# Kernel tuning notes

Measured on AMD Instinct MI355X. Metric: run time of the kernel, lower is better.

The kernel has to match this reference:

```python
import jax, jax.numpy as jnp
import numpy as np

N, NTIMES, D_FEAT = 2048, 32, 128


def setup_inputs() -> dict:
    key = jax.random.key(0)
    k1, k2 = jax.random.split(key)
    return {
        "target_fairness": jnp.zeros((), dtype=jnp.float32),
        "prediction": jax.random.uniform(k1, (N, NTIMES), dtype=jnp.float32),
        "X_distance": jax.random.normal(k2, (N, D_FEAT), dtype=jnp.float32),
        "ntimes": NTIMES,
        "scale": jnp.ones((), dtype=jnp.float32),
    }


def reference(target_fairness, prediction, X_distance, ntimes, scale):
    n = prediction.shape[0]
    # cosine distance matrix: 1 - cos_sim, matches sklearn cosine_distances
    norms = jnp.linalg.norm(X_distance, axis=1, keepdims=True)
    Xn = X_distance / norms
    dist = 1.0 - Xn @ Xn.T  # [N, N]
    # pairwise |pred_j - pred_k| over all time points: [N, N, T]
    diff = jnp.abs(prediction[:, None, :] - prediction[None, :, :])
    hinge = jnp.maximum(0.0, diff - scale * dist[:, :, None])
    # only pairs k > j contribute
    mask = jnp.triu(jnp.ones((n, n), dtype=bool), k=1)
    R_beta = jnp.sum(jnp.where(mask[:, :, None], hinge, 0.0))
    model_fairness = 2.0 * R_beta / (n * (n - 1) * ntimes)
    return jnp.maximum(0.0, model_fairness - target_fairness)
```

## Files before the change

kernel.cpp:

```cpp
#include <hip/hip_runtime.h>

#define N 2048
#define T 32
#define D 128
#define BT 32
#define MT (N / BT)
#define NTILES (MT * (MT + 1) / 2)
#define STR 36

#define LGKM0() __builtin_amdgcn_s_waitcnt(0xc07f)

__global__ __launch_bounds__(64) void pair_kernel(
    const float* __restrict__ pred,
    const float* __restrict__ X,
    const float* __restrict__ scale_p,
    double* __restrict__ partials) {
  __shared__ float SA[BT * STR], SB[BT * STR];
  __shared__ float nrmA[BT], nrmB[BT];

  const int t = blockIdx.x;
  int a = (int)((2 * MT + 1 -
                 sqrtf((float)((2 * MT + 1) * (2 * MT + 1) - 8 * t))) * 0.5f);
  while (a > 0 && t < a * MT - a * (a - 1) / 2) --a;
  while (t >= (a + 1) * MT - (a + 1) * a / 2) ++a;
  const int b = a + (t - (a * MT - a * (a - 1) / 2));

  const int tid  = threadIdx.x;
  const int srow = tid >> 1;
  const int co   = (tid & 1) << 4;
  const int aRow0 = a * BT, bRow0 = b * BT;
  const float scale = scale_p[0];

  const float* xar = X + (size_t)(aRow0 + srow) * D + co;
  const float* xbr = X + (size_t)(bRow0 + srow) * D + co;

  const int tx = tid & 7, ty = tid >> 3;
  float dot[4][4];
#pragma unroll
  for (int i = 0; i < 4; ++i)
#pragma unroll
    for (int l = 0; l < 4; ++l) dot[i][l] = 0.0f;
  float ssA = 0.0f, ssB = 0.0f;

  for (int dc = 0; dc < 4; ++dc) {
#pragma unroll
    for (int j = 0; j < 4; ++j) {
      float4 va = *(const float4*)(xar + dc * 32 + 4 * j);
      float4 vb = *(const float4*)(xbr + dc * 32 + 4 * j);
      ssA += va.x * va.x + va.y * va.y + va.z * va.z + va.w * va.w;
      ssB += vb.x * vb.x + vb.y * vb.y + vb.z * vb.z + vb.w * vb.w;
      *(float4*)(&SA[srow * STR + co + 4 * j]) = va;
      *(float4*)(&SB[srow * STR + co + 4 * j]) = vb;
    }
    LGKM0();
#pragma unroll
    for (int d4 = 0; d4 < 8; ++d4) {
      float4 a4[4], b4[4];
#pragma unroll
      for (int i = 0; i < 4; ++i) {
        a4[i] = *(const float4*)(&SA[(ty + 8 * i) * STR + d4 * 4]);
        b4[i] = *(const float4*)(&SB[(tx + 8 * i) * STR + d4 * 4]);
      }
#pragma unroll
      for (int i = 0; i < 4; ++i)
#pragma unroll
        for (int l = 0; l < 4; ++l)
          dot[i][l] += a4[i].x * b4[l].x + a4[i].y * b4[l].y +
                       a4[i].z * b4[l].z + a4[i].w * b4[l].w;
    }
  }

  ssA += __shfl_xor(ssA, 1, 64);
  ssB += __shfl_xor(ssB, 1, 64);
  if ((tid & 1) == 0) {
    nrmA[srow] = rsqrtf(ssA);
    nrmB[srow] = rsqrtf(ssB);
  }

  {
    const float* par = pred + (size_t)(aRow0 + srow) * T + co;
    const float* pbr = pred + (size_t)(bRow0 + srow) * T + co;
#pragma unroll
    for (int j = 0; j < 4; ++j) {
      *(float4*)(&SA[srow * STR + co + 4 * j]) = *(const float4*)(par + 4 * j);
      *(float4*)(&SB[srow * STR + co + 4 * j]) = *(const float4*)(pbr + 4 * j);
    }
  }
  LGKM0();

  float na[4], nb[4];
#pragma unroll
  for (int i = 0; i < 4; ++i) {
    na[i] = nrmA[ty + 8 * i];
    nb[i] = nrmB[tx + 8 * i];
  }
  float ps[4][4];
#pragma unroll
  for (int i = 0; i < 4; ++i)
#pragma unroll
    for (int l = 0; l < 4; ++l) {
      dot[i][l] = scale * (1.0f - dot[i][l] * na[i] * nb[l]);
      ps[i][l]  = 0.0f;
    }

#pragma unroll
  for (int t4 = 0; t4 < 8; ++t4) {
    float4 qa[4], qb[4];
#pragma unroll
    for (int i = 0; i < 4; ++i) {
      qa[i] = *(const float4*)(&SA[(ty + 8 * i) * STR + t4 * 4]);
      qb[i] = *(const float4*)(&SB[(tx + 8 * i) * STR + t4 * 4]);
    }
#pragma unroll
    for (int i = 0; i < 4; ++i)
#pragma unroll
      for (int l = 0; l < 4; ++l) {
        float s = dot[i][l];
        ps[i][l] += fmaxf(fabsf(qa[i].x - qb[l].x), s) +
                    fmaxf(fabsf(qa[i].y - qb[l].y), s) +
                    fmaxf(fabsf(qa[i].z - qb[l].z), s) +
                    fmaxf(fabsf(qa[i].w - qb[l].w), s);
      }
  }

  float tsum = 0.0f;
  const bool offdiag = (b > a);
#pragma unroll
  for (int i = 0; i < 4; ++i)
#pragma unroll
    for (int l = 0; l < 4; ++l) {
      int jy = ty + 8 * i, kx = tx + 8 * l;
      bool valid = offdiag || (kx > jy);
      tsum += valid ? (ps[i][l] - 32.0f * dot[i][l]) : 0.0f;
    }

  double dsum = (double)tsum;
#pragma unroll
  for (int off = 32; off > 0; off >>= 1) dsum += __shfl_down(dsum, off, 64);
  if (tid == 0) partials[blockIdx.x] = dsum;
}

__global__ __launch_bounds__(256) void finalize_kernel(
    const double* __restrict__ partials, const float* __restrict__ target,
    float* __restrict__ out) {
  __shared__ double red[4];
  double s = 0.0;
  for (int i = threadIdx.x; i < NTILES; i += 256) s += partials[i];
#pragma unroll
  for (int off = 32; off > 0; off >>= 1) s += __shfl_down(s, off, 64);
  int wave = threadIdx.x >> 6, lane = threadIdx.x & 63;
  if (lane == 0) red[wave] = s;
  __syncthreads();
  if (threadIdx.x == 0) {
    double tot = red[0] + red[1] + red[2] + red[3];
    double mf  = 2.0 * tot / ((double)N * (double)(N - 1) * (double)T);
    double r   = mf - (double)target[0];
    out[0] = (float)(r > 0.0 ? r : 0.0);
  }
}

extern "C" void kernel_launch(void* const* d_in, const int* in_sizes, int n_in,
                              void* d_out, int out_size, void* d_ws, size_t ws_size,
                              hipStream_t stream) {
  const float* target = (const float*)d_in[0];
  const float* pred   = (const float*)d_in[1];
  const float* X      = (const float*)d_in[2];
  const float* scale  = (const float*)d_in[4];

  double* partials = (double*)d_ws;

  pair_kernel<<<dim3(NTILES), dim3(64), 0, stream>>>(pred, X, scale, partials);
  finalize_kernel<<<dim3(1), dim3(256), 0, stream>>>(partials, target,
                                                     (float*)d_out);
}
```

Measured before the change: 97.50 us.

## Compute cosine Gram tile with split-bf16 MFMA instead of scalar FMA

Replaces the LDS-staged scalar FP32 dot-product loop for the 32x32 Gram tile with MFMA 16x16x32 bf16 instructions. Each value is split into high and low bf16 parts, and three products (hh, hl, lh) approximate FP32 accuracy. X is read directly from global memory into registers, so the LDS staging and its waits for the feature matrix are gone. The hinge loop is remapped to the MFMA output layout. This trades some dot-product precision and three times the MFMA count for far fewer scalar FMAs.

```diff
diff --git a/kernel.cpp b/kernel.cpp
--- a/kernel.cpp
+++ b/kernel.cpp
@@ -8,14 +8,33 @@
 #define NTILES (MT * (MT + 1) / 2)
 #define STR 36
 
+typedef float floatx4 __attribute__((ext_vector_type(4)));
+typedef short bf16x8 __attribute__((ext_vector_type(8)));
+
 #define LGKM0() __builtin_amdgcn_s_waitcnt(0xc07f)
+
+__device__ __forceinline__ void split8(float4 a, float4 b, bf16x8& h, bf16x8& l) {
+  float v[8] = {a.x, a.y, a.z, a.w, b.x, b.y, b.z, b.w};
+#pragma unroll
+  for (int i = 0; i < 8; ++i) {
+    unsigned u = __float_as_uint(v[i]);
+    h[i] = (short)(u >> 16);
+    float lo = v[i] - __uint_as_float(u & 0xffff0000u);
+    l[i] = (short)(__float_as_uint(lo) >> 16);
+  }
+}
+
+__device__ __forceinline__ float sumsq8(float4 a, float4 b) {
+  return a.x * a.x + a.y * a.y + a.z * a.z + a.w * a.w +
+         b.x * b.x + b.y * b.y + b.z * b.z + b.w * b.w;
+}
 
 __global__ __launch_bounds__(64) void pair_kernel(
     const float* __restrict__ pred,
     const float* __restrict__ X,
     const float* __restrict__ scale_p,
     double* __restrict__ partials) {
-  __shared__ float SA[BT * STR], SB[BT * STR];
+  __shared__ float Pa[BT * STR], Pb[BT * STR];
   __shared__ float nrmA[BT], nrmB[BT];
 
   const int t = blockIdx.x;
@@ -26,113 +45,125 @@
   const int b = a + (t - (a * MT - a * (a - 1) / 2));
 
   const int tid  = threadIdx.x;
-  const int srow = tid >> 1;
-  const int co   = (tid & 1) << 4;
+  const int m    = tid & 15;
+  const int quad = tid >> 4;
   const int aRow0 = a * BT, bRow0 = b * BT;
   const float scale = scale_p[0];
 
-  const float* xar = X + (size_t)(aRow0 + srow) * D + co;
-  const float* xbr = X + (size_t)(bRow0 + srow) * D + co;
-
-  const int tx = tid & 7, ty = tid >> 3;
-  float dot[4][4];
-#pragma unroll
-  for (int i = 0; i < 4; ++i)
-#pragma unroll
-    for (int l = 0; l < 4; ++l) dot[i][l] = 0.0f;
-  float ssA = 0.0f, ssB = 0.0f;
-
-  for (int dc = 0; dc < 4; ++dc) {
-#pragma unroll
-    for (int j = 0; j < 4; ++j) {
-      float4 va = *(const float4*)(xar + dc * 32 + 4 * j);
-      float4 vb = *(const float4*)(xbr + dc * 32 + 4 * j);
-      ssA += va.x * va.x + va.y * va.y + va.z * va.z + va.w * va.w;
-      ssB += vb.x * vb.x + vb.y * vb.y + vb.z * vb.z + vb.w * vb.w;
-      *(float4*)(&SA[srow * STR + co + 4 * j]) = va;
-      *(float4*)(&SB[srow * STR + co + 4 * j]) = vb;
-    }
-    LGKM0();
-#pragma unroll
-    for (int d4 = 0; d4 < 8; ++d4) {
-      float4 a4[4], b4[4];
-#pragma unroll
-      for (int i = 0; i < 4; ++i) {
-        a4[i] = *(const float4*)(&SA[(ty + 8 * i) * STR + d4 * 4]);
-        b4[i] = *(const float4*)(&SB[(tx + 8 * i) * STR + d4 * 4]);
-      }
-#pragma unroll
-      for (int i = 0; i < 4; ++i)
-#pragma unroll
-        for (int l = 0; l < 4; ++l)
-          dot[i][l] += a4[i].x * b4[l].x + a4[i].y * b4[l].y +
-                       a4[i].z * b4[l].z + a4[i].w * b4[l].w;
-    }
-  }
-
-  ssA += __shfl_xor(ssA, 1, 64);
-  ssB += __shfl_xor(ssB, 1, 64);
-  if ((tid & 1) == 0) {
-    nrmA[srow] = rsqrtf(ssA);
-    nrmB[srow] = rsqrtf(ssB);
-  }
-
   {
+    const int srow = tid >> 1, co = (tid & 1) << 4;
     const float* par = pred + (size_t)(aRow0 + srow) * T + co;
     const float* pbr = pred + (size_t)(bRow0 + srow) * T + co;
 #pragma unroll
     for (int j = 0; j < 4; ++j) {
-      *(float4*)(&SA[srow * STR + co + 4 * j]) = *(const float4*)(par + 4 * j);
-      *(float4*)(&SB[srow * STR + co + 4 * j]) = *(const float4*)(pbr + 4 * j);
+      *(float4*)(&Pa[srow * STR + co + 4 * j]) = *(const float4*)(par + 4 * j);
+      *(float4*)(&Pb[srow * STR + co + 4 * j]) = *(const float4*)(pbr + 4 * j);
     }
   }
+
+  floatx4 acc[2][2];
+#pragma unroll
+  for (int I = 0; I < 2; ++I)
+#pragma unroll
+    for (int J = 0; J < 2; ++J) acc[I][J] = (floatx4){0.f, 0.f, 0.f, 0.f};
+  float ssA[2] = {0.f, 0.f}, ssB[2] = {0.f, 0.f};
+
+  const float* xa0 = X + (size_t)(aRow0 + m) * D + quad * 8;
+  const float* xb0 = X + (size_t)(bRow0 + m) * D + quad * 8;
+
+#pragma unroll
+  for (int ks = 0; ks < 4; ++ks) {
+    bf16x8 hA[2], lA[2], hB[2], lB[2];
+#pragma unroll
+    for (int I = 0; I < 2; ++I) {
+      float4 u0 = *(const float4*)(xa0 + (size_t)I * 16 * D + ks * 32);
+      float4 u1 = *(const float4*)(xa0 + (size_t)I * 16 * D + ks * 32 + 4);
+      ssA[I] += sumsq8(u0, u1);
+      split8(u0, u1, hA[I], lA[I]);
+      float4 w0 = *(const float4*)(xb0 + (size_t)I * 16 * D + ks * 32);
+      float4 w1 = *(const float4*)(xb0 + (size_t)I * 16 * D + ks * 32 + 4);
+      ssB[I] += sumsq8(w0, w1);
+      split8(w0, w1, hB[I], lB[I]);
+    }
+#pragma unroll
+    for (int I = 0; I < 2; ++I)
+#pragma unroll
+      for (int J = 0; J < 2; ++J) {
+        acc[I][J] = __builtin_amdgcn_mfma_f32_16x16x32_bf16(hA[I], hB[J],
+                                                            acc[I][J], 0, 0, 0);
+        acc[I][J] = __builtin_amdgcn_mfma_f32_16x16x32_bf16(hA[I], lB[J],
+                                                            acc[I][J], 0, 0, 0);
+        acc[I][J] = __builtin_amdgcn_mfma_f32_16x16x32_bf16(lA[I], hB[J],
+                                                            acc[I][J], 0, 0, 0);
+      }
+  }
+
+#pragma unroll
+  for (int I = 0; I < 2; ++I) {
+    ssA[I] += __shfl_xor(ssA[I], 16, 64);
+    ssA[I] += __shfl_xor(ssA[I], 32, 64);
+    ssB[I] += __shfl_xor(ssB[I], 16, 64);
+    ssB[I] += __shfl_xor(ssB[I], 32, 64);
+  }
+  if (quad == 0) {
+#pragma unroll
+    for (int I = 0; I < 2; ++I) {
+      nrmA[16 * I + m] = rsqrtf(ssA[I]);
+      nrmB[16 * I + m] = rsqrtf(ssB[I]);
+    }
+  }
   LGKM0();
 
-  float na[4], nb[4];
-#pragma unroll
-  for (int i = 0; i < 4; ++i) {
-    na[i] = nrmA[ty + 8 * i];
-    nb[i] = nrmB[tx + 8 * i];
-  }
-  float ps[4][4];
-#pragma unroll
-  for (int i = 0; i < 4; ++i)
-#pragma unroll
-    for (int l = 0; l < 4; ++l) {
-      dot[i][l] = scale * (1.0f - dot[i][l] * na[i] * nb[l]);
-      ps[i][l]  = 0.0f;
-    }
+  float na[2][4], nb[2];
+#pragma unroll
+  for (int I = 0; I < 2; ++I) {
+#pragma unroll
+    for (int r = 0; r < 4; ++r) na[I][r] = nrmA[16 * I + quad * 4 + r];
+    nb[I] = nrmB[16 * I + m];
+  }
+  float sd[2][2][4], ps[2][2][4];
+#pragma unroll
+  for (int I = 0; I < 2; ++I)
+#pragma unroll
+    for (int J = 0; J < 2; ++J)
+#pragma unroll
+      for (int r = 0; r < 4; ++r) {
+        sd[I][J][r] = scale * (1.0f - acc[I][J][r] * na[I][r] * nb[J]);
+        ps[I][J][r] = 0.0f;
+      }
 
 #pragma unroll
   for (int t4 = 0; t4 < 8; ++t4) {
-    float4 qa[4], qb[4];
-#pragma unroll
-    for (int i = 0; i < 4; ++i) {
-      qa[i] = *(const float4*)(&SA[(ty + 8 * i) * STR + t4 * 4]);
-      qb[i] = *(const float4*)(&SB[(tx + 8 * i) * STR + t4 * 4]);
-    }
-#pragma unroll
-    for (int i = 0; i < 4; ++i)
-#pragma unroll
-      for (int l = 0; l < 4; ++l) {
-        float s = dot[i][l];
-        ps[i][l] += fmaxf(fabsf(qa[i].x - qb[l].x), s) +
-                    fmaxf(fabsf(qa[i].y - qb[l].y), s) +
-                    fmaxf(fabsf(qa[i].z - qb[l].z), s) +
-                    fmaxf(fabsf(qa[i].w - qb[l].w), s);
+    float4 qb[2];
+    qb[0] = *(const float4*)(&Pb[m * STR + t4 * 4]);
+    qb[1] = *(const float4*)(&Pb[(16 + m) * STR + t4 * 4]);
+#pragma unroll
+    for (int I = 0; I < 2; ++I)
+#pragma unroll
+      for (int r = 0; r < 4; ++r) {
+        float4 qa = *(const float4*)(&Pa[(16 * I + quad * 4 + r) * STR + t4 * 4]);
+#pragma unroll
+        for (int J = 0; J < 2; ++J) {
+          float s = sd[I][J][r];
+          ps[I][J][r] += fmaxf(fabsf(qa.x - qb[J].x), s) +
+                         fmaxf(fabsf(qa.y - qb[J].y), s) +
+                         fmaxf(fabsf(qa.z - qb[J].z), s) +
+                         fmaxf(fabsf(qa.w - qb[J].w), s);
+        }
       }
   }
 
   float tsum = 0.0f;
-  const bool offdiag = (b > a);
-#pragma unroll
-  for (int i = 0; i < 4; ++i)
-#pragma unroll
-    for (int l = 0; l < 4; ++l) {
-      int jy = ty + 8 * i, kx = tx + 8 * l;
-      bool valid = offdiag || (kx > jy);
-      tsum += valid ? (ps[i][l] - 32.0f * dot[i][l]) : 0.0f;
-    }
+#pragma unroll
+  for (int I = 0; I < 2; ++I)
+#pragma unroll
+    for (int J = 0; J < 2; ++J)
+#pragma unroll
+      for (int r = 0; r < 4; ++r) {
+        int j = aRow0 + 16 * I + quad * 4 + r;
+        int k = bRow0 + 16 * J + m;
+        tsum += (k > j) ? (ps[I][J][r] - 32.0f * sd[I][J][r]) : 0.0f;
+      }
 
   double dsum = (double)tsum;
 #pragma unroll
```

After: 88.09 us. 9.7% less time.
